# Optimization experiments

Measured on AMD Instinct MI355X. Metric: run time of the kernel, lower is better.

Reference implementation:

```python
import jax, jax.numpy as jnp
import numpy as np

H = 16          # num_heads (init kwarg)
EPS = 1e-6      # LayerNorm eps


def rope_freqs(L, d):
    # interleaved RoPE freqs, repeat(f, 'i j -> i (j r)', r=2)
    t = jnp.arange(L, dtype=jnp.float32)
    inv = 1.0 / (10000.0 ** (jnp.arange(0, d, 2, dtype=jnp.float32) / d))
    f = t[:, None] * inv[None, :]          # (L, d//2)
    return jnp.repeat(f, 2, axis=-1)       # (L, d)


def rotate_half(x):
    # pair adjacent elems: (x1, x2) -> (-x2, x1)
    shp = x.shape
    x = x.reshape(shp[:-1] + (shp[-1] // 2, 2))
    x1, x2 = x[..., 0], x[..., 1]
    return jnp.stack((-x2, x1), axis=-1).reshape(shp)


def apply_rope(x, f):
    # x: (B, H, L, d), f: (L, d)
    return x * jnp.cos(f) + rotate_half(x) * jnp.sin(f)


def layernorm(x, g, b):
    m = jnp.mean(x, axis=-1, keepdims=True)
    v = jnp.mean(jnp.square(x - m), axis=-1, keepdims=True)
    return (x - m) * jax.lax.rsqrt(v + EPS) * g + b


def setup_inputs() -> dict:
    key = jax.random.key(0)
    ks = jax.random.split(key, 12)
    B, L, D = 2, 2048, 1024
    Dff = 4 * D
    s = 0.02
    inp = {
        'x': jax.random.normal(ks[0], (B, L, D), jnp.float32),
        'ln1_g': jnp.ones((D,), jnp.float32),
        'ln1_b': jnp.zeros((D,), jnp.float32),
        'wq': jax.random.normal(ks[1], (D, D), jnp.float32) * s,
        'bq': jnp.zeros((D,), jnp.float32),
        'wk': jax.random.normal(ks[2], (D, D), jnp.float32) * s,
        'bk': jnp.zeros((D,), jnp.float32),
        'wv': jax.random.normal(ks[3], (D, D), jnp.float32) * s,
        'bv': jnp.zeros((D,), jnp.float32),
        'wo': jax.random.normal(ks[4], (D, D), jnp.float32) * s,
        'bo': jnp.zeros((D,), jnp.float32),
        'ln2_g': jnp.ones((D,), jnp.float32),
        'ln2_b': jnp.zeros((D,), jnp.float32),
        'w1': jax.random.normal(ks[5], (D, Dff), jnp.float32) * s,
        'b1': jnp.zeros((Dff,), jnp.float32),
        'w2': jax.random.normal(ks[6], (Dff, D), jnp.float32) * s,
        'b2': jnp.zeros((D,), jnp.float32),
        # gates are zero-init in the module; use small random so the block is exercised
        'gate_msa': jax.random.normal(ks[7], (1, 1, D), jnp.float32) * 0.1,
        'gate_mlp': jax.random.normal(ks[8], (1, 1, D), jnp.float32) * 0.1,
    }
    return inp


def reference(x, ln1_g, ln1_b, wq, bq, wk, bk, wv, bv, wo, bo,
              ln2_g, ln2_b, w1, b1, w2, b2, gate_msa, gate_mlp):
    B, L, D = x.shape
    hd = D // H
    # --- self-attention branch ---
    h = layernorm(x, ln1_g, ln1_b)
    q = (h @ wq + bq).reshape(B, L, H, hd).transpose(0, 2, 1, 3)  # (B,H,L,hd)
    k = (h @ wk + bk).reshape(B, L, H, hd).transpose(0, 2, 1, 3)
    v = (h @ wv + bv).reshape(B, L, H, hd).transpose(0, 2, 1, 3)
    f = rope_freqs(L, hd)
    q = apply_rope(q, f)
    k = apply_rope(k, f)
    scores = jnp.einsum('bhic,bhjc->bhij', q, k) / np.float32(np.sqrt(hd))
    attn = jax.nn.softmax(scores, axis=-1)  # dropout disabled (eval)
    o = jnp.einsum('bhij,bhjc->bhic', attn, v)
    o = o.transpose(0, 2, 1, 3).reshape(B, L, D)
    x = x + gate_msa * (o @ wo + bo)
    # --- gated MLP branch ---
    h2 = layernorm(x, ln2_g, ln2_b)
    mlp = jax.nn.gelu(h2 @ w1 + b1, approximate=False) @ w2 + b2
    return x + gate_mlp * mlp
```

## Files before the change

### kernel.cpp

```cpp
#include <hip/hip_runtime.h>

typedef unsigned short u16;
typedef __attribute__((ext_vector_type(4))) float f32x4;
typedef __attribute__((ext_vector_type(16))) float f32x16;
typedef __attribute__((ext_vector_type(8))) short bf16x8;

#define DEV static __device__ __forceinline__

DEV float bf2f(u16 u) { unsigned int i = ((unsigned int)u) << 16; return __builtin_bit_cast(float, i); }
DEV u16 f2bf(float f) {
  unsigned int x = __builtin_bit_cast(unsigned int, f);
  x += 0x7fffu + ((x >> 16) & 1u);
  return (u16)(x >> 16);
}

DEV unsigned cvtpk(float lo, float hi) {
  unsigned r;
  asm("v_cvt_pk_bf16_f32 %0, %1, %2" : "=v"(r) : "v"(lo), "v"(hi));
  return r;
}
DEV float exp2a(float x) {
  float r;
  asm("v_exp_f32 %0, %1" : "=v"(r) : "v"(x));
  return r;
}

template <int N>
DEV void wait_vmcnt() {
  if constexpr (N == 0) asm volatile("s_waitcnt vmcnt(0)" ::: "memory");
  else if constexpr (N == 3) asm volatile("s_waitcnt vmcnt(3)" ::: "memory");
  else if constexpr (N == 4) asm volatile("s_waitcnt vmcnt(4)" ::: "memory");
  else static_assert(N == 0, "unsupported vmcnt");
}

DEV void gload16(const u16* g, u16* l) {
  __builtin_amdgcn_global_load_lds(
      (const __attribute__((address_space(1))) unsigned int*)g,
      (__attribute__((address_space(3))) unsigned int*)l, 16, 0, 0);
}

__global__ __launch_bounds__(256) void ln_k(const float* __restrict__ x,
                                            const float* __restrict__ g,
                                            const float* __restrict__ b,
                                            u16* __restrict__ out) {
  const int row = blockIdx.x;
  const int t = threadIdx.x;
  const float4 v = *(const float4*)(x + (size_t)row * 1024 + t * 4);
  float s = v.x + v.y + v.z + v.w;
  float q = v.x * v.x + v.y * v.y + v.z * v.z + v.w * v.w;
#pragma unroll
  for (int m = 1; m < 64; m <<= 1) { s += __shfl_xor(s, m); q += __shfl_xor(q, m); }
  __shared__ float ss[4], qs[4];
  if ((t & 63) == 0) { ss[t >> 6] = s; qs[t >> 6] = q; }
  __syncthreads();
  s = ss[0] + ss[1] + ss[2] + ss[3];
  q = qs[0] + qs[1] + qs[2] + qs[3];
  const float mean = s * (1.0f / 1024.0f);
  const float var = q * (1.0f / 1024.0f) - mean * mean;
  const float rs = rsqrtf(var + 1e-6f);
  const float4 gv = *(const float4*)(g + t * 4);
  const float4 bv = *(const float4*)(b + t * 4);
  ushort4 o;
  o.x = f2bf((v.x - mean) * rs * gv.x + bv.x);
  o.y = f2bf((v.y - mean) * rs * gv.y + bv.y);
  o.z = f2bf((v.z - mean) * rs * gv.z + bv.z);
  o.w = f2bf((v.w - mean) * rs * gv.w + bv.w);
  *(ushort4*)(out + (size_t)row * 1024 + t * 4) = o;
}

__global__ __launch_bounds__(256) void tcvt_k(const float* __restrict__ src,
                                              u16* __restrict__ dst, int K, int N) {
  __shared__ u16 tl[32][33];
  const int k0 = blockIdx.x * 32, n0 = blockIdx.y * 32;
  const int c = threadIdx.x & 31, r0 = threadIdx.x >> 5;
#pragma unroll
  for (int p = 0; p < 4; p++) {
    const int r = p * 8 + r0;
    tl[r][c] = f2bf(src[(size_t)(k0 + r) * N + n0 + c]);
  }
  __syncthreads();
#pragma unroll
  for (int p = 0; p < 4; p++) {
    const int r = p * 8 + r0;
    dst[(size_t)(n0 + r) * K + k0 + c] = tl[c][r];
  }
}

template <int EPI, int TN>
__global__ __launch_bounds__(256) void gemm_bt(const u16* __restrict__ A,
                                               const u16* __restrict__ Bt,
                                               const float* __restrict__ bias,
                                               const float* __restrict__ resid,
                                               const float* __restrict__ gate,
                                               void* __restrict__ outv,
                                               int M, int N, int K) {
  constexpr int MI = (TN == 128) ? 4 : 2;
  constexpr int WRS = (TN == 128) ? 64 : 32;
  constexpr int L = 2 + TN / 64;
  __shared__ __align__(16) u16 lA[3][128 * 32];
  __shared__ __align__(16) u16 lB[3][TN * 32];
  const int tid = threadIdx.x;
  const int lane = tid & 63, wid = tid >> 6;
  const int l4 = lane >> 4, l15 = lane & 15;
  const int wr = (TN == 128) ? (wid >> 1) : wid;
  const int wc = (TN == 128) ? (wid & 1) : 0;
  const int mBase = blockIdx.x * 128;
  const int nBase = blockIdx.y * TN;

  f32x4 acc[MI][4];
#pragma unroll
  for (int i = 0; i < MI; i++)
#pragma unroll
    for (int j = 0; j < 4; j++)
#pragma unroll
      for (int e = 0; e < 4; e++) acc[i][j][e] = 0.f;

  const int sRow = tid >> 2;
  const int sCol = (((tid & 3) ^ ((sRow >> 1) & 3))) * 8;
  const int rsw = (l15 >> 1) & 3;

#define STAGE(bufi, k0)                                                               \
  {                                                                                   \
    _Pragma("unroll") for (int p = 0; p < 2; p++)                                     \
        gload16(A + (size_t)(mBase + p * 64 + sRow) * K + (k0) + sCol,                \
                &lA[bufi][p * 2048 + wid * 512]);                                     \
    _Pragma("unroll") for (int p = 0; p < TN / 64; p++)                               \
        gload16(Bt + (size_t)(nBase + p * 64 + sRow) * K + (k0) + sCol,               \
                &lB[bufi][p * 2048 + wid * 512]);                                     \
  }

  const int nt = K >> 5;
  STAGE(0, 0);
  STAGE(1, 32);
  wait_vmcnt<L>();
  __builtin_amdgcn_s_barrier();
  __builtin_amdgcn_sched_barrier(0);

  int bsel = 0;
  for (int it = 0; it < nt; ++it) {
    bf16x8 af[MI], bfr[4];
#pragma unroll
    for (int mi = 0; mi < MI; mi++)
      af[mi] = *(const bf16x8*)(&lA[bsel][(wr * WRS + mi * 16 + l15) * 32 + (l4 ^ rsw) * 8]);
#pragma unroll
    for (int ni = 0; ni < 4; ni++)
      bfr[ni] = *(const bf16x8*)(&lB[bsel][(wc * 64 + ni * 16 + l15) * 32 + (l4 ^ rsw) * 8]);
    if (it + 2 < nt) {
      int b2 = bsel + 2; if (b2 >= 3) b2 -= 3;
      STAGE(b2, (it + 2) * 32);
    }
#pragma unroll
    for (int mi = 0; mi < MI; mi++)
#pragma unroll
      for (int ni = 0; ni < 4; ni++)
        acc[mi][ni] = __builtin_amdgcn_mfma_f32_16x16x32_bf16(af[mi], bfr[ni], acc[mi][ni], 0, 0, 0);
    if (it + 1 < nt) {
      asm volatile("s_waitcnt lgkmcnt(0)" ::: "memory");
      __builtin_amdgcn_sched_barrier(0);
      if (it + 2 < nt) wait_vmcnt<L>();
      else wait_vmcnt<0>();
      __builtin_amdgcn_s_barrier();
      __builtin_amdgcn_sched_barrier(0);
    }
    bsel = (bsel == 2) ? 0 : bsel + 1;
  }
#undef STAGE

  u16* obf = (u16*)outv;
  float* of = (float*)outv;
#pragma unroll
  for (int mi = 0; mi < MI; mi++) {
#pragma unroll
    for (int ni = 0; ni < 4; ni++) {
      const int row0 = mBase + wr * WRS + mi * 16 + l4 * 4;
      const int col = nBase + wc * 64 + ni * 16 + l15;
      const float bb = bias[col];
#pragma unroll
      for (int r = 0; r < 4; r++) {
        const float v = acc[mi][ni][r] + bb;
        const size_t idx = (size_t)(row0 + r) * N + col;
        if (EPI == 0) {
          obf[idx] = f2bf(v);
        } else if (EPI == 1) {
          const float ge = 0.5f * v * (1.0f + erff(v * 0.70710678118654752f));
          obf[idx] = f2bf(ge);
        } else if (EPI == 2) {
          of[idx] = resid[idx] + gate[col] * v;
        } else {
          of[idx] = of[idx] + gate[col] * v;
        }
      }
    }
  }
}

__global__ __launch_bounds__(256) void rope_k(const u16* __restrict__ qkv,
                                              u16* __restrict__ qr, u16* __restrict__ kr) {
  const int sel = blockIdx.y;
  const int rid = blockIdx.x * 8 + (threadIdx.x >> 5);
  const int i = threadIdx.x & 31;
  const int b = rid >> 15;
  const int h = (rid >> 11) & 15;
  const int t = rid & 2047;
  const u16* src = qkv + (size_t)(b * 2048 + t) * 3072 + sel * 1024 + h * 64 + 2 * i;
  const ushort2 uv = *(const ushort2*)src;
  const float x0 = bf2f(uv.x), x1 = bf2f(uv.y);
  const float inv = __expf(-(float)i * 0.28782313662425572f);
  float sn, cs;
  sincosf((float)t * inv, &sn, &cs);
  const float sc = sel ? 1.0f : 0.18033688011112042f;
  ushort2 ov;
  ov.x = f2bf((x0 * cs - x1 * sn) * sc);
  ov.y = f2bf((x1 * cs + x0 * sn) * sc);
  *(ushort2*)((sel ? kr : qr) + (size_t)rid * 64 + 2 * i) = ov;
}

__global__ __launch_bounds__(256) void vtrans_k(const u16* __restrict__ qkv, u16* __restrict__ vt) {
  __shared__ u16 tl[64][65];
  const int bh = blockIdx.x >> 5;
  const int t0 = (blockIdx.x & 31) * 64;
  const int b = bh >> 4, h = bh & 15;
  const int tid = threadIdx.x;
#pragma unroll
  for (int p = 0; p < 16; p++) {
    const int e = p * 256 + tid;
    const int tr = e >> 6, d = e & 63;
    tl[tr][d] = qkv[(size_t)(b * 2048 + t0 + tr) * 3072 + 2048 + h * 64 + d];
  }
  __syncthreads();
#pragma unroll
  for (int p = 0; p < 16; p++) {
    const int e = p * 256 + tid;
    const int dr = e >> 6, tc = e & 63;
    vt[(size_t)(bh * 64 + dr) * 2048 + t0 + tc] = tl[tc][dr];
  }
}

__global__ __launch_bounds__(512) void attn_k(const u16* __restrict__ q,
                                              const u16* __restrict__ k,
                                              const u16* __restrict__ vt,
                                              u16* __restrict__ o) {
  const int bh = blockIdx.y;
  const int tid = threadIdx.x;
  const int grp = tid >> 8;
  const int wid = (tid >> 6) & 3;
  const int lane = tid & 63;
  const int h = lane >> 5, rq = lane & 31;
  const int qrow0 = blockIdx.x * 128 + wid * 32;

  __shared__ __align__(16) u16 kls[2][2][4096];
  __shared__ __align__(16) u16 vls[2][2][4096];
  __shared__ __align__(16) float alds[8][32];
  __shared__ __align__(16) float mls[4][32], lls[4][32];

  const u16* qbase = q + ((size_t)bh * 2048 + qrow0 + rq) * 64 + 8 * h;
  bf16x8 qf[4];
#pragma unroll
  for (int db = 0; db < 4; db++) qf[db] = *(const bf16x8*)(qbase + db * 16);

  float m0 = -1e30f, ls0 = 0.f;
  f32x16 oacc0, oacc1;
#pragma unroll
  for (int e = 0; e < 16; e++) { oacc0[e] = 0.f; oacc1[e] = 0.f; }

  const char* kg = (const char*)(k + (size_t)bh * 2048 * 64);
  const char* vg = (const char*)(vt + (size_t)bh * 64 * 2048);
  const int t8 = tid & 255;
  const int sA = t8, sB = 256 + t8;
  const int rA = sA >> 3, cA = ((sA & 7) ^ (rA & 7)) << 4;
  const int rB = sB >> 3, cB = ((sB & 7) ^ (rB & 7)) << 4;
  u16* kgrp = &kls[grp][0][0];
  u16* vgrp = &vls[grp][0][0];
  u16* kd0 = kgrp + wid * 512;
  u16* kd1 = kgrp + 2048 + wid * 512;
  u16* vd0 = vgrp + wid * 512;
  u16* vd1 = vgrp + 2048 + wid * 512;
  const int kvbase = grp * 1024;

#define STAGE(bufi, kv0)                                                            \
  {                                                                                 \
    const int _o = (bufi)*4096;                                                     \
    gload16((const u16*)(kg + (size_t)((kv0) + rA) * 128 + cA), kd0 + _o);          \
    gload16((const u16*)(kg + (size_t)((kv0) + rB) * 128 + cB), kd1 + _o);          \
    gload16((const u16*)(vg + (size_t)rA * 4096 + (kv0)*2 + cA), vd0 + _o);         \
    gload16((const u16*)(vg + (size_t)rB * 4096 + (kv0)*2 + cB), vd1 + _o);         \
  }

  STAGE(0, kvbase);
  __syncthreads();

  float* AL = alds[tid >> 6];
  const int swz = (rq & 7) << 4;

#define PACK8(S, B, OUT)                                                            \
  {                                                                                 \
    unsigned wA = cvtpk(S[B + 0], S[B + 1]), wB_ = cvtpk(S[B + 2], S[B + 3]);       \
    unsigned wC = cvtpk(S[B + 4], S[B + 5]), wD = cvtpk(S[B + 6], S[B + 7]);        \
    unsigned xA = __shfl_xor(wA, 32), xB = __shfl_xor(wB_, 32);                     \
    unsigned xC = __shfl_xor(wC, 32), xD = __shfl_xor(wD, 32);                      \
    union { unsigned u[4]; bf16x8 v; } _m;                                          \
    _m.u[0] = h ? xC : wA; _m.u[1] = h ? xD : wB_;                                  \
    _m.u[2] = h ? wC : xA; _m.u[3] = h ? wD : xB;                                   \
    OUT = _m.v;                                                                     \
  }

  int buf = 0;
  for (int it = 0; it < 16; ++it) {
    if (it < 15) STAGE(buf ^ 1, kvbase + (it + 1) * 64);
    const char* K = (const char*)(kgrp + buf * 4096);
    const char* V = (const char*)(vgrp + buf * 4096);

    f32x16 st0, st1;
#pragma unroll
    for (int e = 0; e < 16; e++) { st0[e] = 0.f; st1[e] = 0.f; }
#pragma unroll
    for (int db = 0; db < 4; db++) {
      const int cb = db * 32;
      const bf16x8 ka0 = *(const bf16x8*)(K + rq * 128 + ((cb + 16 * h) ^ swz));
      const bf16x8 ka1 = *(const bf16x8*)(K + (32 + rq) * 128 + ((cb + 16 * h) ^ swz));
      st0 = __builtin_amdgcn_mfma_f32_32x32x16_bf16(ka0, qf[db], st0, 0, 0, 0);
      st1 = __builtin_amdgcn_mfma_f32_32x32x16_bf16(ka1, qf[db], st1, 0, 0, 0);
    }

    float t0 = fmaxf(fmaxf(st0[0], st0[1]), fmaxf(st0[2], st0[3]));
    float t1 = fmaxf(fmaxf(st0[4], st0[5]), fmaxf(st0[6], st0[7]));
    float t2 = fmaxf(fmaxf(st0[8], st0[9]), fmaxf(st0[10], st0[11]));
    float t3 = fmaxf(fmaxf(st0[12], st0[13]), fmaxf(st0[14], st0[15]));
    float t4 = fmaxf(fmaxf(st1[0], st1[1]), fmaxf(st1[2], st1[3]));
    float t5 = fmaxf(fmaxf(st1[4], st1[5]), fmaxf(st1[6], st1[7]));
    float t6 = fmaxf(fmaxf(st1[8], st1[9]), fmaxf(st1[10], st1[11]));
    float t7 = fmaxf(fmaxf(st1[12], st1[13]), fmaxf(st1[14], st1[15]));
    float pm = fmaxf(fmaxf(fmaxf(t0, t1), fmaxf(t2, t3)), fmaxf(fmaxf(t4, t5), fmaxf(t6, t7)));
    pm = fmaxf(pm, __shfl_xor(pm, 32));
    const bool need = !__all(pm <= m0 + 11.54f);
    float al0 = 1.0f;
    if (need) {
      const float mn = fmaxf(m0, pm);
      al0 = exp2a(m0 - mn);
      m0 = mn;
    }
#pragma unroll
    for (int e = 0; e < 16; e++) {
      st0[e] = exp2a(st0[e] - m0);
      st1[e] = exp2a(st1[e] - m0);
    }
    float u0 = (st0[0] + st0[1]) + (st0[2] + st0[3]);
    float u1 = (st0[4] + st0[5]) + (st0[6] + st0[7]);
    float u2 = (st0[8] + st0[9]) + (st0[10] + st0[11]);
    float u3 = (st0[12] + st0[13]) + (st0[14] + st0[15]);
    float u4 = (st1[0] + st1[1]) + (st1[2] + st1[3]);
    float u5 = (st1[4] + st1[5]) + (st1[6] + st1[7]);
    float u6 = (st1[8] + st1[9]) + (st1[10] + st1[11]);
    float u7 = (st1[12] + st1[13]) + (st1[14] + st1[15]);
    float ps = ((u0 + u1) + (u2 + u3)) + ((u4 + u5) + (u6 + u7));
    ps += __shfl_xor(ps, 32);
    ls0 = ls0 * al0 + ps;

    if (need) {
      if (lane < 32) AL[rq] = al0;
      const f32x4 a0 = *(const f32x4*)((const char*)AL + 16 * h);
      const f32x4 a1 = *(const f32x4*)((const char*)AL + 32 + 16 * h);
      const f32x4 a2 = *(const f32x4*)((const char*)AL + 64 + 16 * h);
      const f32x4 a3 = *(const f32x4*)((const char*)AL + 96 + 16 * h);
#pragma unroll
      for (int r = 0; r < 4; r++) {
        oacc0[r] *= a0[r]; oacc0[4 + r] *= a1[r]; oacc0[8 + r] *= a2[r]; oacc0[12 + r] *= a3[r];
        oacc1[r] *= a0[r]; oacc1[4 + r] *= a1[r]; oacc1[8 + r] *= a2[r]; oacc1[12 + r] *= a3[r];
      }
    }

    bf16x8 pa[4];
    PACK8(st0, 0, pa[0]);
    PACK8(st0, 8, pa[1]);
    PACK8(st1, 0, pa[2]);
    PACK8(st1, 8, pa[3]);

#pragma unroll
    for (int kb = 0; kb < 4; kb++) {
      const int cb = kb * 32;
      const bf16x8 vb0 = *(const bf16x8*)(V + rq * 128 + ((cb + 16 * h) ^ swz));
      const bf16x8 vb1 = *(const bf16x8*)(V + (32 + rq) * 128 + ((cb + 16 * h) ^ swz));
      oacc0 = __builtin_amdgcn_mfma_f32_32x32x16_bf16(pa[kb], vb0, oacc0, 0, 0, 0);
      oacc1 = __builtin_amdgcn_mfma_f32_32x32x16_bf16(pa[kb], vb1, oacc1, 0, 0, 0);
    }
    __syncthreads();
    buf ^= 1;
  }
#undef STAGE
#undef PACK8

  float* comb = (float*)&kls[0][0][0];
  if (grp == 1) {
    if (lane < 32) { mls[wid][rq] = m0; lls[wid][rq] = ls0; }
    float* cw = comb + wid * 2048;
#pragma unroll
    for (int r = 0; r < 16; r++) {
      const int ql = (r & 3) + 8 * (r >> 2) + 4 * h;
      cw[ql * 64 + rq] = oacc0[r];
      cw[ql * 64 + 32 + rq] = oacc1[r];
    }
  }
  __syncthreads();
  if (grp == 0) {
    const float mb = mls[wid][rq], lb = lls[wid][rq];
    const float M = fmaxf(m0, mb);
    const float sa = exp2a(m0 - M), sb = exp2a(mb - M);
    const float linv = 1.0f / (ls0 * sa + lb * sb);
    if (lane < 32) { AL[rq] = sa * linv; mls[wid][rq] = sb * linv; }
    asm volatile("s_waitcnt lgkmcnt(0)" ::: "memory");
    f32x4 fa[4], fb[4];
#pragma unroll
    for (int g = 0; g < 4; g++) {
      fa[g] = *(const f32x4*)((const char*)AL + g * 32 + 16 * h);
      fb[g] = *(const f32x4*)((const char*)&mls[wid][0] + g * 32 + 16 * h);
    }
    const float* cw = comb + wid * 2048;
    const int b = bh >> 4, hh = bh & 15;
#pragma unroll
    for (int r = 0; r < 16; r++) {
      const int ql = (r & 3) + 8 * (r >> 2) + 4 * h;
      const float A = fa[r >> 2][r & 3], B = fb[r >> 2][r & 3];
      u16* orow = o + ((size_t)b * 2048 + qrow0 + ql) * 1024 + hh * 64;
      orow[rq] = f2bf(oacc0[r] * A + cw[ql * 64 + rq] * B);
      orow[32 + rq] = f2bf(oacc1[r] * A + cw[ql * 64 + 32 + rq] * B);
    }
  }
}

extern "C" void kernel_launch(void* const* d_in, const int* in_sizes, int n_in,
                              void* d_out, int out_size, void* d_ws, size_t ws_size,
                              hipStream_t stream) {
  (void)in_sizes; (void)n_in; (void)out_size; (void)ws_size;
  const float* x     = (const float*)d_in[0];
  const float* ln1_g = (const float*)d_in[1];
  const float* ln1_b = (const float*)d_in[2];
  const float* wq    = (const float*)d_in[3];
  const float* bq    = (const float*)d_in[4];
  const float* wk    = (const float*)d_in[5];
  const float* bk    = (const float*)d_in[6];
  const float* wv    = (const float*)d_in[7];
  const float* bv    = (const float*)d_in[8];
  const float* wo    = (const float*)d_in[9];
  const float* bo    = (const float*)d_in[10];
  const float* ln2_g = (const float*)d_in[11];
  const float* ln2_b = (const float*)d_in[12];
  const float* w1    = (const float*)d_in[13];
  const float* b1    = (const float*)d_in[14];
  const float* w2    = (const float*)d_in[15];
  const float* b2    = (const float*)d_in[16];
  const float* gmsa  = (const float*)d_in[17];
  const float* gmlp  = (const float*)d_in[18];
  float* out = (float*)d_out;

  char* w = (char*)d_ws;
  auto alloc = [&](size_t bytes) {
    char* p = w;
    w += (bytes + 255) & ~(size_t)255;
    return p;
  };
  u16* h1     = (u16*)alloc(4096UL * 1024 * 2);
  u16* wqkv_t = (u16*)alloc(3072UL * 1024 * 2);
  u16* wo_t   = (u16*)alloc(1024UL * 1024 * 2);
  u16* w1_t   = (u16*)alloc(4096UL * 1024 * 2);
  u16* w2_t   = (u16*)alloc(1024UL * 4096 * 2);
  float* bqkv = (float*)alloc(3072UL * 4);
  u16* qkv    = (u16*)alloc(4096UL * 3072 * 2);
  u16* q_r    = (u16*)alloc(65536UL * 64 * 2);
  u16* k_r    = (u16*)alloc(65536UL * 64 * 2);
  u16* v_t    = (u16*)alloc(65536UL * 64 * 2);
  u16* o_at   = (u16*)alloc(4096UL * 1024 * 2);
  u16* h2     = (u16*)alloc(4096UL * 1024 * 2);
  u16* g1     = (u16*)alloc(4096UL * 4096 * 2);

  tcvt_k<<<dim3(32, 32), 256, 0, stream>>>(wq, wqkv_t, 1024, 1024);
  tcvt_k<<<dim3(32, 32), 256, 0, stream>>>(wk, wqkv_t + 1024 * 1024, 1024, 1024);
  tcvt_k<<<dim3(32, 32), 256, 0, stream>>>(wv, wqkv_t + 2048 * 1024, 1024, 1024);
  tcvt_k<<<dim3(32, 32), 256, 0, stream>>>(wo, wo_t, 1024, 1024);
  tcvt_k<<<dim3(32, 128), 256, 0, stream>>>(w1, w1_t, 1024, 4096);
  tcvt_k<<<dim3(128, 32), 256, 0, stream>>>(w2, w2_t, 4096, 1024);
  hipMemcpyAsync(bqkv,        bq, 1024 * sizeof(float), hipMemcpyDeviceToDevice, stream);
  hipMemcpyAsync(bqkv + 1024, bk, 1024 * sizeof(float), hipMemcpyDeviceToDevice, stream);
  hipMemcpyAsync(bqkv + 2048, bv, 1024 * sizeof(float), hipMemcpyDeviceToDevice, stream);

  ln_k<<<4096, 256, 0, stream>>>(x, ln1_g, ln1_b, h1);
  gemm_bt<0, 128><<<dim3(32, 24), 256, 0, stream>>>(h1, wqkv_t, bqkv, nullptr, nullptr, qkv, 4096, 3072, 1024);
  rope_k<<<dim3(8192, 2), 256, 0, stream>>>(qkv, q_r, k_r);
  vtrans_k<<<1024, 256, 0, stream>>>(qkv, v_t);
  attn_k<<<dim3(16, 32), 512, 0, stream>>>(q_r, k_r, v_t, o_at);
  gemm_bt<2, 64><<<dim3(32, 16), 256, 0, stream>>>(o_at, wo_t, bo, x, gmsa, out, 4096, 1024, 1024);

  ln_k<<<4096, 256, 0, stream>>>(out, ln2_g, ln2_b, h2);
  gemm_bt<1, 128><<<dim3(32, 32), 256, 0, stream>>>(h2, w1_t, b1, nullptr, nullptr, g1, 4096, 4096, 1024);
  gemm_bt<3, 64><<<dim3(32, 16), 256, 0, stream>>>(g1, w2_t, b2, nullptr, gmlp, out, 4096, 1024, 4096);
}
```

Baseline: 284.1 us.

## Split K across two warp groups in the narrow-N output GEMMs

Adds a 512-thread GEMM kernel for the N=1024 projections (wo and w2) in which two groups of four waves each accumulate half of K into separate LDS pipelines. Group 1 then writes its partial accumulators to shared memory and group 0 reduces them before the gated residual epilogue. The goal is more waves per output tile, giving better latency hiding and more MFMA issue for these 512-block launches. The cost is double the LDS footprint per block, an extra LDS reduction pass, and fewer resident blocks per CU. The general GEMM template is reduced to the fixed 128x128 tile.

```diff
diff --git a/kernel.cpp b/kernel.cpp
--- a/kernel.cpp
+++ b/kernel.cpp
@@ -86,30 +86,25 @@
   }
 }
 
-template <int EPI, int TN>
+template <int EPI>
 __global__ __launch_bounds__(256) void gemm_bt(const u16* __restrict__ A,
                                                const u16* __restrict__ Bt,
                                                const float* __restrict__ bias,
-                                               const float* __restrict__ resid,
-                                               const float* __restrict__ gate,
                                                void* __restrict__ outv,
                                                int M, int N, int K) {
-  constexpr int MI = (TN == 128) ? 4 : 2;
-  constexpr int WRS = (TN == 128) ? 64 : 32;
-  constexpr int L = 2 + TN / 64;
+  constexpr int L = 4;
   __shared__ __align__(16) u16 lA[3][128 * 32];
-  __shared__ __align__(16) u16 lB[3][TN * 32];
+  __shared__ __align__(16) u16 lB[3][128 * 32];
   const int tid = threadIdx.x;
   const int lane = tid & 63, wid = tid >> 6;
   const int l4 = lane >> 4, l15 = lane & 15;
-  const int wr = (TN == 128) ? (wid >> 1) : wid;
-  const int wc = (TN == 128) ? (wid & 1) : 0;
+  const int wr = wid >> 1, wc = wid & 1;
   const int mBase = blockIdx.x * 128;
-  const int nBase = blockIdx.y * TN;
-
-  f32x4 acc[MI][4];
-#pragma unroll
-  for (int i = 0; i < MI; i++)
+  const int nBase = blockIdx.y * 128;
+
+  f32x4 acc[4][4];
+#pragma unroll
+  for (int i = 0; i < 4; i++)
 #pragma unroll
     for (int j = 0; j < 4; j++)
 #pragma unroll
@@ -123,10 +118,10 @@
   {                                                                                   \
     _Pragma("unroll") for (int p = 0; p < 2; p++)                                     \
         gload16(A + (size_t)(mBase + p * 64 + sRow) * K + (k0) + sCol,                \
-                &lA[bufi][p * 2048 + wid * 512]);                                     \
-    _Pragma("unroll") for (int p = 0; p < TN / 64; p++)                               \
+                &lA[bufi][p * 2048 + tid * 8]);                                       \
+    _Pragma("unroll") for (int p = 0; p < 2; p++)                                     \
         gload16(Bt + (size_t)(nBase + p * 64 + sRow) * K + (k0) + sCol,               \
-                &lB[bufi][p * 2048 + wid * 512]);                                     \
+                &lB[bufi][p * 2048 + tid * 8]);                                       \
   }
 
   const int nt = K >> 5;
@@ -138,10 +133,10 @@
 
   int bsel = 0;
   for (int it = 0; it < nt; ++it) {
-    bf16x8 af[MI], bfr[4];
-#pragma unroll
-    for (int mi = 0; mi < MI; mi++)
-      af[mi] = *(const bf16x8*)(&lA[bsel][(wr * WRS + mi * 16 + l15) * 32 + (l4 ^ rsw) * 8]);
+    bf16x8 af[4], bfr[4];
+#pragma unroll
+    for (int mi = 0; mi < 4; mi++)
+      af[mi] = *(const bf16x8*)(&lA[bsel][(wr * 64 + mi * 16 + l15) * 32 + (l4 ^ rsw) * 8]);
 #pragma unroll
     for (int ni = 0; ni < 4; ni++)
       bfr[ni] = *(const bf16x8*)(&lB[bsel][(wc * 64 + ni * 16 + l15) * 32 + (l4 ^ rsw) * 8]);
@@ -150,7 +145,7 @@
       STAGE(b2, (it + 2) * 32);
     }
 #pragma unroll
-    for (int mi = 0; mi < MI; mi++)
+    for (int mi = 0; mi < 4; mi++)
 #pragma unroll
       for (int ni = 0; ni < 4; ni++)
         acc[mi][ni] = __builtin_amdgcn_mfma_f32_16x16x32_bf16(af[mi], bfr[ni], acc[mi][ni], 0, 0, 0);
@@ -167,12 +162,11 @@
 #undef STAGE
 
   u16* obf = (u16*)outv;
-  float* of = (float*)outv;
-#pragma unroll
-  for (int mi = 0; mi < MI; mi++) {
+#pragma unroll
+  for (int mi = 0; mi < 4; mi++) {
 #pragma unroll
     for (int ni = 0; ni < 4; ni++) {
-      const int row0 = mBase + wr * WRS + mi * 16 + l4 * 4;
+      const int row0 = mBase + wr * 64 + mi * 16 + l4 * 4;
       const int col = nBase + wc * 64 + ni * 16 + l15;
       const float bb = bias[col];
 #pragma unroll
@@ -181,13 +175,125 @@
         const size_t idx = (size_t)(row0 + r) * N + col;
         if (EPI == 0) {
           obf[idx] = f2bf(v);
-        } else if (EPI == 1) {
+        } else {
           const float ge = 0.5f * v * (1.0f + erff(v * 0.70710678118654752f));
           obf[idx] = f2bf(ge);
-        } else if (EPI == 2) {
-          of[idx] = resid[idx] + gate[col] * v;
-        } else {
-          of[idx] = of[idx] + gate[col] * v;
+        }
+      }
+    }
+  }
+}
+
+template <int EPI>
+__global__ __launch_bounds__(512) void gemm_sk(const u16* __restrict__ A,
+                                               const u16* __restrict__ Bt,
+                                               const float* __restrict__ bias,
+                                               const float* __restrict__ resid,
+                                               const float* __restrict__ gate,
+                                               float* __restrict__ outv,
+                                               int M, int N, int K) {
+  constexpr int L = 3;
+  __shared__ __align__(16) u16 lA[2][3][128 * 32];
+  __shared__ __align__(16) u16 lB[2][3][64 * 32];
+  const int tid = threadIdx.x;
+  const int grp = tid >> 8;
+  const int t8 = tid & 255;
+  const int lane = tid & 63;
+  const int wid4 = (tid >> 6) & 3;
+  const int l4 = lane >> 4, l15 = lane & 15;
+  const int mBase = blockIdx.x * 128;
+  const int nBase = blockIdx.y * 64;
+  const int Kh = K >> 1;
+  const int kbase = grp * Kh;
+
+  f32x4 acc[2][4];
+#pragma unroll
+  for (int i = 0; i < 2; i++)
+#pragma unroll
+    for (int j = 0; j < 4; j++)
+#pragma unroll
+      for (int e = 0; e < 4; e++) acc[i][j][e] = 0.f;
+
+  const int sRow = t8 >> 2;
+  const int sCol = (((t8 & 3) ^ ((sRow >> 1) & 3))) * 8;
+  const int rsw = (l15 >> 1) & 3;
+
+#define STAGE(bufi, k0)                                                                  \
+  {                                                                                      \
+    _Pragma("unroll") for (int p = 0; p < 2; p++)                                        \
+        gload16(A + (size_t)(mBase + p * 64 + sRow) * K + kbase + (k0) + sCol,           \
+                &lA[grp][bufi][p * 2048 + t8 * 8]);                                      \
+    gload16(Bt + (size_t)(nBase + sRow) * K + kbase + (k0) + sCol,                       \
+            &lB[grp][bufi][t8 * 8]);                                                     \
+  }
+
+  const int nt = Kh >> 5;
+  STAGE(0, 0);
+  STAGE(1, 32);
+  wait_vmcnt<L>();
+  __builtin_amdgcn_s_barrier();
+  __builtin_amdgcn_sched_barrier(0);
+
+  int bsel = 0;
+  for (int it = 0; it < nt; ++it) {
+    bf16x8 af[2], bfr[4];
+#pragma unroll
+    for (int mi = 0; mi < 2; mi++)
+      af[mi] = *(const bf16x8*)(&lA[grp][bsel][(wid4 * 32 + mi * 16 + l15) * 32 + (l4 ^ rsw) * 8]);
+#pragma unroll
+    for (int ni = 0; ni < 4; ni++)
+      bfr[ni] = *(const bf16x8*)(&lB[grp][bsel][(ni * 16 + l15) * 32 + (l4 ^ rsw) * 8]);
+    if (it + 2 < nt) {
+      int b2 = bsel + 2; if (b2 >= 3) b2 -= 3;
+      STAGE(b2, (it + 2) * 32);
+    }
+#pragma unroll
+    for (int mi = 0; mi < 2; mi++)
+#pragma unroll
+      for (int ni = 0; ni < 4; ni++)
+        acc[mi][ni] = __builtin_amdgcn_mfma_f32_16x16x32_bf16(af[mi], bfr[ni], acc[mi][ni], 0, 0, 0);
+    if (it + 1 < nt) {
+      asm volatile("s_waitcnt lgkmcnt(0)" ::: "memory");
+      __builtin_amdgcn_sched_barrier(0);
+      if (it + 2 < nt) wait_vmcnt<L>();
+      else wait_vmcnt<0>();
+      __builtin_amdgcn_s_barrier();
+      __builtin_amdgcn_sched_barrier(0);
+    }
+    bsel = (bsel == 2) ? 0 : bsel + 1;
+  }
+#undef STAGE
+
+  __syncthreads();
+  float* comb = (float*)&lA[0][0][0];
+  if (grp == 1) {
+#pragma unroll
+    for (int mi = 0; mi < 2; mi++)
+#pragma unroll
+      for (int ni = 0; ni < 4; ni++)
+#pragma unroll
+        for (int r = 0; r < 4; r++) {
+          const int e = (mi * 4 + ni) * 4 + r;
+          comb[wid4 * 2048 + e * 64 + lane] = acc[mi][ni][r];
+        }
+  }
+  __syncthreads();
+  if (grp == 0) {
+#pragma unroll
+    for (int mi = 0; mi < 2; mi++) {
+#pragma unroll
+      for (int ni = 0; ni < 4; ni++) {
+        const int row0 = mBase + wid4 * 32 + mi * 16 + l4 * 4;
+        const int col = nBase + ni * 16 + l15;
+        const float bb = bias[col];
+        const float gg = gate[col];
+#pragma unroll
+        for (int r = 0; r < 4; r++) {
+          const int e = (mi * 4 + ni) * 4 + r;
+          const float v = acc[mi][ni][r] + comb[wid4 * 2048 + e * 64 + lane] + bb;
+          const size_t idx = (size_t)(row0 + r) * N + col;
+          if (EPI == 2) outv[idx] = resid[idx] + gg * v;
+          else outv[idx] = outv[idx] + gg * v;
         }
       }
     }
@@ -483,13 +589,13 @@
   hipMemcpyAsync(bqkv + 2048, bv, 1024 * sizeof(float), hipMemcpyDeviceToDevice, stream);
 
   ln_k<<<4096, 256, 0, stream>>>(x, ln1_g, ln1_b, h1);
-  gemm_bt<0, 128><<<dim3(32, 24), 256, 0, stream>>>(h1, wqkv_t, bqkv, nullptr, nullptr, qkv, 4096, 3072, 1024);
+  gemm_bt<0><<<dim3(32, 24), 256, 0, stream>>>(h1, wqkv_t, bqkv, qkv, 4096, 3072, 1024);
   rope_k<<<dim3(8192, 2), 256, 0, stream>>>(qkv, q_r, k_r);
   vtrans_k<<<1024, 256, 0, stream>>>(qkv, v_t);
   attn_k<<<dim3(16, 32), 512, 0, stream>>>(q_r, k_r, v_t, o_at);
-  gemm_bt<2, 64><<<dim3(32, 16), 256, 0, stream>>>(o_at, wo_t, bo, x, gmsa, out, 4096, 1024, 1024);
+  gemm_sk<2><<<dim3(32, 16), 512, 0, stream>>>(o_at, wo_t, bo, x, gmsa, out, 4096, 1024, 1024);
 
   ln_k<<<4096, 256, 0, stream>>>(out, ln2_g, ln2_b, h2);
-  gemm_bt<1, 128><<<dim3(32, 32), 256, 0, stream>>>(h2, w1_t, b1, nullptr, nullptr, g1, 4096, 4096, 1024);
-  gemm_bt<3, 64><<<dim3(32, 16), 256, 0, stream>>>(g1, w2_t, b2, nullptr, gmlp, out, 4096, 1024, 4096);
-}
+  gemm_bt<1><<<dim3(32, 32), 256, 0, stream>>>(h2, w1_t, b1, g1, 4096, 4096, 1024);
+  gemm_sk<3><<<dim3(32, 16), 512, 0, stream>>>(g1, w2_t, b2, nullptr, gmlp, out, 4096, 1024, 4096);
+}
```

Result: slower. 290.4 us (+2.2%).

## Split-K the output GEMMs with atomic accumulation and raise MFMA priority in attention

Applied to the files above, without the earlier changes.

The Wo and W2 GEMMs now use a new gemm_at kernel that splits K in two across blockIdx.z, doubling the block count from 512 to 1024 so more CUs are kept busy. Each half atomically adds its gated partial into an output buffer that is first initialised with x via a device memcpy; only the z=0 half adds the bias. The attention kernel also wraps its MFMA loops in s_setprio raises. In exchange, the change adds an extra 16MB copy, float atomics (which make summation order nondeterministic), and read-modify-write traffic on the output.

```diff
diff --git a/kernel.cpp b/kernel.cpp
--- a/kernel.cpp
+++ b/kernel.cpp
@@ -90,8 +90,6 @@
 __global__ __launch_bounds__(256) void gemm_bt(const u16* __restrict__ A,
                                                const u16* __restrict__ Bt,
                                                const float* __restrict__ bias,
-                                               const float* __restrict__ resid,
-                                               const float* __restrict__ gate,
                                                void* __restrict__ outv,
                                                int M, int N, int K) {
   constexpr int MI = (TN == 128) ? 4 : 2;
@@ -167,7 +165,6 @@
 #undef STAGE
 
   u16* obf = (u16*)outv;
-  float* of = (float*)outv;
 #pragma unroll
   for (int mi = 0; mi < MI; mi++) {
 #pragma unroll
@@ -181,14 +178,103 @@
         const size_t idx = (size_t)(row0 + r) * N + col;
         if (EPI == 0) {
           obf[idx] = f2bf(v);
-        } else if (EPI == 1) {
+        } else {
           const float ge = 0.5f * v * (1.0f + erff(v * 0.70710678118654752f));
           obf[idx] = f2bf(ge);
-        } else if (EPI == 2) {
-          of[idx] = resid[idx] + gate[col] * v;
-        } else {
-          of[idx] = of[idx] + gate[col] * v;
         }
+      }
+    }
+  }
+}
+
+__global__ __launch_bounds__(256) void gemm_at(const u16* __restrict__ A,
+                                               const u16* __restrict__ Bt,
+                                               const float* __restrict__ bias,
+                                               const float* __restrict__ gate,
+                                               float* __restrict__ outv,
+                                               int M, int N, int K) {
+  constexpr int L = 3;
+  __shared__ __align__(16) u16 lA[3][128 * 32];
+  __shared__ __align__(16) u16 lB[3][64 * 32];
+  const int tid = threadIdx.x;
+  const int lane = tid & 63, wid = tid >> 6;
+  const int l4 = lane >> 4, l15 = lane & 15;
+  const int mBase = blockIdx.x * 128;
+  const int nBase = blockIdx.y * 64;
+  const int Kh = K >> 1;
+  const int kbase = blockIdx.z * Kh;
+
+  f32x4 acc[2][4];
+#pragma unroll
+  for (int i = 0; i < 2; i++)
+#pragma unroll
+    for (int j = 0; j < 4; j++)
+#pragma unroll
+      for (int e = 0; e < 4; e++) acc[i][j][e] = 0.f;
+
+  const int sRow = tid >> 2;
+  const int sCol = (((tid & 3) ^ ((sRow >> 1) & 3))) * 8;
+  const int rsw = (l15 >> 1) & 3;
+
+#define STAGE(bufi, k0)                                                               \
+  {                                                                                   \
+    _Pragma("unroll") for (int p = 0; p < 2; p++)                                     \
+        gload16(A + (size_t)(mBase + p * 64 + sRow) * K + kbase + (k0) + sCol,        \
+                &lA[bufi][p * 2048 + wid * 512]);                                     \
+    gload16(Bt + (size_t)(nBase + sRow) * K + kbase + (k0) + sCol,                    \
+            &lB[bufi][wid * 512]);                                                    \
+  }
+
+  const int nt = Kh >> 5;
+  STAGE(0, 0);
+  STAGE(1, 32);
+  wait_vmcnt<L>();
+  __builtin_amdgcn_s_barrier();
+  __builtin_amdgcn_sched_barrier(0);
+
+  int bsel = 0;
+  for (int it = 0; it < nt; ++it) {
+    bf16x8 af[2], bfr[4];
+#pragma unroll
+    for (int mi = 0; mi < 2; mi++)
+      af[mi] = *(const bf16x8*)(&lA[bsel][(wid * 32 + mi * 16 + l15) * 32 + (l4 ^ rsw) * 8]);
+#pragma unroll
+    for (int ni = 0; ni < 4; ni++)
+      bfr[ni] = *(const bf16x8*)(&lB[bsel][(ni * 16 + l15) * 32 + (l4 ^ rsw) * 8]);
+    if (it + 2 < nt) {
+      int b2 = bsel + 2; if (b2 >= 3) b2 -= 3;
+      STAGE(b2, (it + 2) * 32);
+    }
+#pragma unroll
+    for (int mi = 0; mi < 2; mi++)
+#pragma unroll
+      for (int ni = 0; ni < 4; ni++)
+        acc[mi][ni] = __builtin_amdgcn_mfma_f32_16x16x32_bf16(af[mi], bfr[ni], acc[mi][ni], 0, 0, 0);
+    if (it + 1 < nt) {
+      asm volatile("s_waitcnt lgkmcnt(0)" ::: "memory");
+      __builtin_amdgcn_sched_barrier(0);
+      if (it + 2 < nt) wait_vmcnt<L>();
+      else wait_vmcnt<0>();
+      __builtin_amdgcn_s_barrier();
+      __builtin_amdgcn_sched_barrier(0);
+    }
+    bsel = (bsel == 2) ? 0 : bsel + 1;
+  }
+#undef STAGE
+
+  const float bsc = (blockIdx.z == 0) ? 1.0f : 0.0f;
+#pragma unroll
+  for (int mi = 0; mi < 2; mi++) {
+#pragma unroll
+    for (int ni = 0; ni < 4; ni++) {
+      const int row0 = mBase + wid * 32 + mi * 16 + l4 * 4;
+      const int col = nBase + ni * 16 + l15;
+      const float bb = bias[col] * bsc;
+      const float gg = gate[col];
+#pragma unroll
+      for (int r = 0; r < 4; r++) {
+        const size_t idx = (size_t)(row0 + r) * N + col;
+        atomicAdd(&outv[idx], gg * (acc[mi][ni][r] + bb));
       }
     }
   }
@@ -313,6 +399,7 @@
     f32x16 st0, st1;
 #pragma unroll
     for (int e = 0; e < 16; e++) { st0[e] = 0.f; st1[e] = 0.f; }
+    __builtin_amdgcn_s_setprio(1);
 #pragma unroll
     for (int db = 0; db < 4; db++) {
       const int cb = db * 32;
@@ -321,6 +408,7 @@
       st0 = __builtin_amdgcn_mfma_f32_32x32x16_bf16(ka0, qf[db], st0, 0, 0, 0);
       st1 = __builtin_amdgcn_mfma_f32_32x32x16_bf16(ka1, qf[db], st1, 0, 0, 0);
     }
+    __builtin_amdgcn_s_setprio(0);
 
     float t0 = fmaxf(fmaxf(st0[0], st0[1]), fmaxf(st0[2], st0[3]));
     float t1 = fmaxf(fmaxf(st0[4], st0[5]), fmaxf(st0[6], st0[7]));
@@ -375,6 +463,7 @@
     PACK8(st1, 0, pa[2]);
     PACK8(st1, 8, pa[3]);
 
+    __builtin_amdgcn_s_setprio(1);
 #pragma unroll
     for (int kb = 0; kb < 4; kb++) {
       const int cb = kb * 32;
@@ -383,6 +472,7 @@
       oacc0 = __builtin_amdgcn_mfma_f32_32x32x16_bf16(pa[kb], vb0, oacc0, 0, 0, 0);
       oacc1 = __builtin_amdgcn_mfma_f32_32x32x16_bf16(pa[kb], vb1, oacc1, 0, 0, 0);
     }
+    __builtin_amdgcn_s_setprio(0);
     __syncthreads();
     buf ^= 1;
   }
@@ -483,13 +573,14 @@
   hipMemcpyAsync(bqkv + 2048, bv, 1024 * sizeof(float), hipMemcpyDeviceToDevice, stream);
 
   ln_k<<<4096, 256, 0, stream>>>(x, ln1_g, ln1_b, h1);
-  gemm_bt<0, 128><<<dim3(32, 24), 256, 0, stream>>>(h1, wqkv_t, bqkv, nullptr, nullptr, qkv, 4096, 3072, 1024);
+  gemm_bt<0, 128><<<dim3(32, 24), 256, 0, stream>>>(h1, wqkv_t, bqkv, qkv, 4096, 3072, 1024);
   rope_k<<<dim3(8192, 2), 256, 0, stream>>>(qkv, q_r, k_r);
   vtrans_k<<<1024, 256, 0, stream>>>(qkv, v_t);
   attn_k<<<dim3(16, 32), 512, 0, stream>>>(q_r, k_r, v_t, o_at);
-  gemm_bt<2, 64><<<dim3(32, 16), 256, 0, stream>>>(o_at, wo_t, bo, x, gmsa, out, 4096, 1024, 1024);
+  hipMemcpyAsync(out, x, 4096UL * 1024 * sizeof(float), hipMemcpyDeviceToDevice, stream);
+  gemm_at<<<dim3(32, 16, 2), 256, 0, stream>>>(o_at, wo_t, bo, gmsa, out, 4096, 1024, 1024);
 
   ln_k<<<4096, 256, 0, stream>>>(out, ln2_g, ln2_b, h2);
-  gemm_bt<1, 128><<<dim3(32, 32), 256, 0, stream>>>(h2, w1_t, b1, nullptr, nullptr, g1, 4096, 4096, 1024);
-  gemm_bt<3, 64><<<dim3(32, 16), 256, 0, stream>>>(g1, w2_t, b2, nullptr, gmlp, out, 4096, 1024, 4096);
-}
+  gemm_bt<1, 128><<<dim3(32, 32), 256, 0, stream>>>(h2, w1_t, b1, g1, 4096, 4096, 1024);
+  gemm_at<<<dim3(32, 16, 2), 256, 0, stream>>>(g1, w2_t, b2, gmlp, out, 4096, 1024, 4096);
+}
```

Result: slower. 328.5 us (+15.6%).
